# Performance work log

Hardware: AMD Instinct MI355X
Metric: run time of the kernel (lower is better)

Reference implementation:

```python
import jax, jax.numpy as jnp
import numpy as np

N_NODES = 50000
N_EDGES = 800000
D_IN = 64
D_OUT = 64


def setup_inputs() -> dict:
    key = jax.random.key(0)
    k1, k2, k3, k4, k5, k6 = jax.random.split(key, 6)
    stdv = 1.0 / np.sqrt(D_OUT)
    return {
        "X": jax.random.normal(k1, (N_NODES, D_IN), dtype=jnp.float32),
        "edge_src": jax.random.randint(k2, (N_EDGES,), 0, N_NODES, dtype=jnp.int32),
        "edge_dst": jax.random.randint(k3, (N_EDGES,), 0, N_NODES, dtype=jnp.int32),
        "edge_weight": jax.random.uniform(k4, (N_EDGES,), dtype=jnp.float32),
        "weight": jax.random.uniform(k5, (D_IN, D_OUT), jnp.float32, -stdv, stdv),
        "b": jax.random.uniform(k6, (D_OUT,), jnp.float32, -stdv, stdv),
    }


def reference(X, edge_src, edge_dst, edge_weight, weight, b):
    # support = X @ W                        [N, D_OUT]
    support = jnp.dot(X, weight)
    # spmm: out[d] = sum_{e: dst(e)=d} w_e * support[src(e)]
    messages = edge_weight[:, None] * support[edge_src]  # [E, D_OUT]
    output = jax.ops.segment_sum(messages, edge_dst, num_segments=N_NODES)
    return output + b
```

## Files before the change

kernel.cpp:

```cpp
#include <hip/hip_runtime.h>
#include <hip/hip_bf16.h>

#define N_NODES 50000
#define N_EDGES 800000
#define DIM     64
#define CAP     64

#define GEMM_BLOCKS ((N_NODES + 31) / 32)
#define FILL_BLOCKS ((N_EDGES / 4 + 255) / 256)
#define TOTAL_BLOCKS (GEMM_BLOCKS + FILL_BLOCKS)
#define INTERLEAVED  (2 * FILL_BLOCKS)

#define WS_SUPPORT  0
#define WS_CURSOR   6400000
#define WS_BUCKET   9600000

__device__ inline unsigned bf16_hi(float f) {
    const unsigned u = __float_as_uint(f);
    return (u + 0x7fffu + ((u >> 16) & 1u)) & 0xffff0000u;
}

__global__ __launch_bounds__(256) void fused_gemm_fill_kernel(
        const float* __restrict__ X,
        const float* __restrict__ W,
        ushort* __restrict__ support,
        const int*   __restrict__ edge_src,
        const int*   __restrict__ edge_dst,
        const float* __restrict__ edge_weight,
        int*      __restrict__ cursor,
        unsigned* __restrict__ bucket) {
    const int tid = threadIdx.x;

    if (blockIdx.x < INTERLEAVED && (blockIdx.x & 1) == 0) {
        const int bid  = blockIdx.x >> 1;
        const int base = (bid * 256 + tid) * 4;
        if (base < N_EDGES) {
            const int4   d = *(const int4*)  &edge_dst[base];
            const int4   s = *(const int4*)  &edge_src[base];
            const float4 w = *(const float4*)&edge_weight[base];
            const unsigned e0 = bf16_hi(w.x) | (unsigned)s.x;
            const unsigned e1 = bf16_hi(w.y) | (unsigned)s.y;
            const unsigned e2 = bf16_hi(w.z) | (unsigned)s.z;
            const unsigned e3 = bf16_hi(w.w) | (unsigned)s.w;
            const int p0 = atomicAdd(&cursor[d.x << 4], 1);
            const int p1 = atomicAdd(&cursor[d.y << 4], 1);
            const int p2 = atomicAdd(&cursor[d.z << 4], 1);
            const int p3 = atomicAdd(&cursor[d.w << 4], 1);
            if (p0 < CAP) bucket[d.x * CAP + p0] = e0;
            if (p1 < CAP) bucket[d.y * CAP + p1] = e1;
            if (p2 < CAP) bucket[d.z * CAP + p2] = e2;
            if (p3 < CAP) bucket[d.w * CAP + p3] = e3;
        }
        return;
    }

    __shared__ float sX[32 * 68];
    __shared__ float sW[64 * 64];
    const int bid = (blockIdx.x < INTERLEAVED) ? (blockIdx.x >> 1)
                                               : (blockIdx.x - FILL_BLOCKS);
    const int rowBase = bid * 32;

    #pragma unroll
    for (int i = 0; i < 2; ++i) {
        const int q   = tid + 256 * i;
        const int row = q >> 4;
        const int c4  = q & 15;
        float4 v = make_float4(0.f, 0.f, 0.f, 0.f);
        if (rowBase + row < N_NODES)
            v = *(const float4*)&X[(rowBase + row) * DIM + c4 * 4];
        *(float4*)&sX[row * 68 + c4 * 4] = v;
    }
    #pragma unroll
    for (int i = 0; i < 4; ++i) {
        const int q   = tid + 256 * i;
        const int row = q >> 4;
        const int c4  = q & 15;
        *(float4*)&sW[row * 64 + c4 * 4] = *(const float4*)&W[row * DIM + c4 * 4];
    }
    __syncthreads();

    const int tx = tid & 15;
    const int ty = tid >> 4;
    float acc[2][4];
    #pragma unroll
    for (int i = 0; i < 2; ++i)
        #pragma unroll
        for (int j = 0; j < 4; ++j) acc[i][j] = 0.f;

    #pragma unroll
    for (int k4 = 0; k4 < 16; ++k4) {
        float4 xv[2], wv[4];
        #pragma unroll
        for (int i = 0; i < 2; ++i)
            xv[i] = *(const float4*)&sX[(ty * 2 + i) * 68 + k4 * 4];
        #pragma unroll
        for (int kk = 0; kk < 4; ++kk)
            wv[kk] = *(const float4*)&sW[(k4 * 4 + kk) * 64 + tx * 4];
        #pragma unroll
        for (int i = 0; i < 2; ++i) {
            #pragma unroll
            for (int kk = 0; kk < 4; ++kk) {
                const float f = ((const float*)&xv[i])[kk];
                acc[i][0] += f * wv[kk].x;
                acc[i][1] += f * wv[kk].y;
                acc[i][2] += f * wv[kk].z;
                acc[i][3] += f * wv[kk].w;
            }
        }
    }

    #pragma unroll
    for (int i = 0; i < 2; ++i) {
        const int r = rowBase + ty * 2 + i;
        if (r < N_NODES) {
            ushort4 v;
            v.x = __hip_bfloat16_raw(__float2bfloat16(acc[i][0])).x;
            v.y = __hip_bfloat16_raw(__float2bfloat16(acc[i][1])).x;
            v.z = __hip_bfloat16_raw(__float2bfloat16(acc[i][2])).x;
            v.w = __hip_bfloat16_raw(__float2bfloat16(acc[i][3])).x;
            *(ushort4*)&support[r * DIM + tx * 4] = v;
        }
    }
}

__global__ __launch_bounds__(256) void gather_kernel(const int*      __restrict__ cursor,
                                                     const unsigned* __restrict__ bucket,
                                                     const unsigned* __restrict__ support32,
                                                     const float*    __restrict__ b,
                                                     float* __restrict__ out) {
    const int node = blockIdx.x * 4 + (threadIdx.x >> 6);
    const int lane = threadIdx.x & 63;
    const int half = lane >> 5;
    const int sub  = lane & 31;
    if (node >= N_NODES) return;

    int cnt = cursor[node << 4];
    if (cnt > CAP) cnt = CAP;
    const unsigned ent = bucket[node * CAP + lane];

    float acc0 = 0.f, acc1 = 0.f;
    int j = 0;
    for (; j + 8 <= cnt; j += 8) {
        unsigned e[4], u[4];
        #pragma unroll
        for (int k = 0; k < 4; ++k) e[k] = __shfl(ent, j + 2 * k + half);
        #pragma unroll
        for (int k = 0; k < 4; ++k) u[k] = support32[(e[k] & 0xffffu) * 32 + sub];
        #pragma unroll
        for (int k = 0; k < 4; ++k) {
            const float w = __uint_as_float(e[k] & 0xffff0000u);
            acc0 += w * __uint_as_float(u[k] << 16);
            acc1 += w * __uint_as_float(u[k] & 0xffff0000u);
        }
    }
    for (; j + 2 <= cnt; j += 2) {
        const unsigned e = __shfl(ent, j + half);
        const unsigned u = support32[(e & 0xffffu) * 32 + sub];
        const float    w = __uint_as_float(e & 0xffff0000u);
        acc0 += w * __uint_as_float(u << 16);
        acc1 += w * __uint_as_float(u & 0xffff0000u);
    }
    if (j < cnt) {
        const unsigned e = __shfl(ent, j);
        const unsigned u = support32[(e & 0xffffu) * 32 + sub];
        const float    w = half ? 0.f : __uint_as_float(e & 0xffff0000u);
        acc0 += w * __uint_as_float(u << 16);
        acc1 += w * __uint_as_float(u & 0xffff0000u);
    }

    acc0 += __shfl_xor(acc0, 32);
    acc1 += __shfl_xor(acc1, 32);

    if (half == 0) {
        const float2 bb = *(const float2*)&b[sub * 2];
        float2 o;
        o.x = acc0 + bb.x;
        o.y = acc1 + bb.y;
        *(float2*)&out[node * DIM + sub * 2] = o;
    }
}

extern "C" void kernel_launch(void* const* d_in, const int* in_sizes, int n_in,
                              void* d_out, int out_size, void* d_ws, size_t ws_size,
                              hipStream_t stream) {
    const float* X           = (const float*)d_in[0];
    const int*   edge_src    = (const int*)  d_in[1];
    const int*   edge_dst    = (const int*)  d_in[2];
    const float* edge_weight = (const float*)d_in[3];
    const float* W           = (const float*)d_in[4];
    const float* b           = (const float*)d_in[5];
    float*       out         = (float*)d_out;

    char* ws = (char*)d_ws;
    ushort*   support = (ushort*)  (ws + WS_SUPPORT);
    int*      cursor  = (int*)     (ws + WS_CURSOR);
    unsigned* bucket  = (unsigned*)(ws + WS_BUCKET);

    hipMemsetAsync(cursor, 0, N_NODES * 16 * sizeof(int), stream);

    hipLaunchKernelGGL(fused_gemm_fill_kernel, dim3(TOTAL_BLOCKS),
                       dim3(256), 0, stream,
                       X, W, support, edge_src, edge_dst, edge_weight,
                       cursor, bucket);

    hipLaunchKernelGGL(gather_kernel, dim3(N_NODES / 4), dim3(256), 0, stream,
                       cursor, bucket, (const unsigned*)support, b, out);
}
```

Measured before the change: 143.8 us.

## Merge memset, GEMM/fill and gather into one cooperative persistent kernel

Replaces the memset plus two kernel launches with a single cooperative kernel of 512 persistent blocks. The blocks zero the cursor array, grid-sync, loop over edge-fill chunks and 16-row GEMM tiles, grid-sync again, then run the gather. The cursor array is no longer padded to 64 bytes per node, so it shrinks and its atomics land on adjacent cache lines. The change removes launch gaps and tail effects, but adds the cost of grid-wide barriers, a fixed grid size that may underfill the GPU, and smaller GEMM tiles that reload W per block.

```diff
diff --git a/kernel.cpp b/kernel.cpp
--- a/kernel.cpp
+++ b/kernel.cpp
@@ -1,75 +1,51 @@
 #include <hip/hip_runtime.h>
+#include <hip/hip_cooperative_groups.h>
 #include <hip/hip_bf16.h>
+
+namespace cg = cooperative_groups;
 
 #define N_NODES 50000
 #define N_EDGES 800000
 #define DIM     64
 #define CAP     64
 
-#define GEMM_BLOCKS ((N_NODES + 31) / 32)
-#define FILL_BLOCKS ((N_EDGES / 4 + 255) / 256)
-#define TOTAL_BLOCKS (GEMM_BLOCKS + FILL_BLOCKS)
-#define INTERLEAVED  (2 * FILL_BLOCKS)
+#define GRID_BLOCKS  512
+#define FILL_CHUNKS  ((N_EDGES + 1023) / 1024)
+#define GEMM_TILES   (N_NODES / 16)
+#define PHASEA_WORK  (FILL_CHUNKS + GEMM_TILES)
+#define GATHER_GROUPS (N_NODES / 4)
 
-#define WS_SUPPORT  0
-#define WS_CURSOR   6400000
-#define WS_BUCKET   9600000
+#define WS_SUPPORT 0
+#define WS_CURSOR  6400000
+#define WS_BUCKET  6600192
 
 __device__ inline unsigned bf16_hi(float f) {
     const unsigned u = __float_as_uint(f);
     return (u + 0x7fffu + ((u >> 16) & 1u)) & 0xffff0000u;
 }
 
-__global__ __launch_bounds__(256) void fused_gemm_fill_kernel(
+__global__ __launch_bounds__(256) void mega_kernel(
         const float* __restrict__ X,
         const float* __restrict__ W,
-        ushort* __restrict__ support,
+        ushort*      __restrict__ support,
         const int*   __restrict__ edge_src,
         const int*   __restrict__ edge_dst,
         const float* __restrict__ edge_weight,
-        int*      __restrict__ cursor,
-        unsigned* __restrict__ bucket) {
+        int*         __restrict__ cursor,
+        unsigned*    __restrict__ bucket,
+        const float* __restrict__ b,
+        float*       __restrict__ out) {
+    cg::grid_group grid = cg::this_grid();
     const int tid = threadIdx.x;
 
-    if (blockIdx.x < INTERLEAVED && (blockIdx.x & 1) == 0) {
-        const int bid  = blockIdx.x >> 1;
-        const int base = (bid * 256 + tid) * 4;
-        if (base < N_EDGES) {
-            const int4   d = *(const int4*)  &edge_dst[base];
-            const int4   s = *(const int4*)  &edge_src[base];
-            const float4 w = *(const float4*)&edge_weight[base];
-            const unsigned e0 = bf16_hi(w.x) | (unsigned)s.x;
-            const unsigned e1 = bf16_hi(w.y) | (unsigned)s.y;
-            const unsigned e2 = bf16_hi(w.z) | (unsigned)s.z;
-            const unsigned e3 = bf16_hi(w.w) | (unsigned)s.w;
-            const int p0 = atomicAdd(&cursor[d.x << 4], 1);
-            const int p1 = atomicAdd(&cursor[d.y << 4], 1);
-            const int p2 = atomicAdd(&cursor[d.z << 4], 1);
-            const int p3 = atomicAdd(&cursor[d.w << 4], 1);
-            if (p0 < CAP) bucket[d.x * CAP + p0] = e0;
-            if (p1 < CAP) bucket[d.y * CAP + p1] = e1;
-            if (p2 < CAP) bucket[d.z * CAP + p2] = e2;
-            if (p3 < CAP) bucket[d.w * CAP + p3] = e3;
-        }
-        return;
+    {
+        const int i = blockIdx.x * 256 + tid;
+        if (i < N_NODES) cursor[i] = 0;
     }
+    grid.sync();
 
-    __shared__ float sX[32 * 68];
+    __shared__ float sX[16 * 68];
     __shared__ float sW[64 * 64];
-    const int bid = (blockIdx.x < INTERLEAVED) ? (blockIdx.x >> 1)
-                                               : (blockIdx.x - FILL_BLOCKS);
-    const int rowBase = bid * 32;
-
-    #pragma unroll
-    for (int i = 0; i < 2; ++i) {
-        const int q   = tid + 256 * i;
-        const int row = q >> 4;
-        const int c4  = q & 15;
-        float4 v = make_float4(0.f, 0.f, 0.f, 0.f);
-        if (rowBase + row < N_NODES)
-            v = *(const float4*)&X[(rowBase + row) * DIM + c4 * 4];
-        *(float4*)&sX[row * 68 + c4 * 4] = v;
-    }
     #pragma unroll
     for (int i = 0; i < 4; ++i) {
         const int q   = tid + 256 * i;
@@ -79,104 +55,115 @@
     }
     __syncthreads();
 
-    const int tx = tid & 15;
-    const int ty = tid >> 4;
-    float acc[2][4];
-    #pragma unroll
-    for (int i = 0; i < 2; ++i)
-        #pragma unroll
-        for (int j = 0; j < 4; ++j) acc[i][j] = 0.f;
+    for (int w = blockIdx.x; w < PHASEA_WORK; w += GRID_BLOCKS) {
+        if (w < FILL_CHUNKS) {
+            const int base = w * 1024 + tid * 4;
+            if (base < N_EDGES) {
+                const int4   d = *(const int4*)  &edge_dst[base];
+                const int4   s = *(const int4*)  &edge_src[base];
+                const float4 wt = *(const float4*)&edge_weight[base];
+                const unsigned e0 = bf16_hi(wt.x) | (unsigned)s.x;
+                const unsigned e1 = bf16_hi(wt.y) | (unsigned)s.y;
+                const unsigned e2 = bf16_hi(wt.z) | (unsigned)s.z;
+                const unsigned e3 = bf16_hi(wt.w) | (unsigned)s.w;
+                const int p0 = atomicAdd(&cursor[d.x], 1);
+                const int p1 = atomicAdd(&cursor[d.y], 1);
+                const int p2 = atomicAdd(&cursor[d.z], 1);
+                const int p3 = atomicAdd(&cursor[d.w], 1);
+                if (p0 < CAP) bucket[d.x * CAP + p0] = e0;
+                if (p1 < CAP) bucket[d.y * CAP + p1] = e1;
+                if (p2 < CAP) bucket[d.z * CAP + p2] = e2;
+                if (p3 < CAP) bucket[d.w * CAP + p3] = e3;
+            }
+        } else {
+            const int rowBase = (w - FILL_CHUNKS) * 16;
+            __syncthreads();
+            {
+                const int row = tid >> 4;
+                const int c4  = tid & 15;
+                *(float4*)&sX[row * 68 + c4 * 4] =
+                    *(const float4*)&X[(rowBase + row) * DIM + c4 * 4];
+            }
+            __syncthreads();
 
-    #pragma unroll
-    for (int k4 = 0; k4 < 16; ++k4) {
-        float4 xv[2], wv[4];
-        #pragma unroll
-        for (int i = 0; i < 2; ++i)
-            xv[i] = *(const float4*)&sX[(ty * 2 + i) * 68 + k4 * 4];
-        #pragma unroll
-        for (int kk = 0; kk < 4; ++kk)
-            wv[kk] = *(const float4*)&sW[(k4 * 4 + kk) * 64 + tx * 4];
-        #pragma unroll
-        for (int i = 0; i < 2; ++i) {
+            const int tx = tid & 15;
+            const int ty = tid >> 4;
+            float a0 = 0.f, a1 = 0.f, a2 = 0.f, a3 = 0.f;
             #pragma unroll
-            for (int kk = 0; kk < 4; ++kk) {
-                const float f = ((const float*)&xv[i])[kk];
-                acc[i][0] += f * wv[kk].x;
-                acc[i][1] += f * wv[kk].y;
-                acc[i][2] += f * wv[kk].z;
-                acc[i][3] += f * wv[kk].w;
+            for (int k4 = 0; k4 < 16; ++k4) {
+                const float4 xv = *(const float4*)&sX[ty * 68 + k4 * 4];
+                #pragma unroll
+                for (int kk = 0; kk < 4; ++kk) {
+                    const float4 wv = *(const float4*)&sW[(k4 * 4 + kk) * 64 + tx * 4];
+                    const float  f  = ((const float*)&xv)[kk];
+                    a0 += f * wv.x;
+                    a1 += f * wv.y;
+                    a2 += f * wv.z;
+                    a3 += f * wv.w;
+                }
+            }
+            ushort4 v;
+            v.x = __hip_bfloat16_raw(__float2bfloat16(a0)).x;
+            v.y = __hip_bfloat16_raw(__float2bfloat16(a1)).x;
+            v.z = __hip_bfloat16_raw(__float2bfloat16(a2)).x;
+            v.w = __hip_bfloat16_raw(__float2bfloat16(a3)).x;
+            *(ushort4*)&support[(rowBase + ty) * DIM + tx * 4] = v;
+        }
+    }
+    grid.sync();
+
+    const int lane = tid & 63;
+    const int half = lane >> 5;
+    const int sub  = lane & 31;
+    const unsigned* support32 = (const unsigned*)support;
+    const float2 bb = *(const float2*)&b[sub * 2];
+
+    for (int g = blockIdx.x; g < GATHER_GROUPS; g += GRID_BLOCKS) {
+        const int node = g * 4 + (tid >> 6);
+
+        int cnt = cursor[node];
+        if (cnt > CAP) cnt = CAP;
+        const unsigned ent = bucket[node * CAP + lane];
+
+        float acc0 = 0.f, acc1 = 0.f;
+        int j = 0;
+        for (; j + 8 <= cnt; j += 8) {
+            unsigned e[4], u[4];
+            #pragma unroll
+            for (int k = 0; k < 4; ++k) e[k] = __shfl(ent, j + 2 * k + half);
+            #pragma unroll
+            for (int k = 0; k < 4; ++k) u[k] = support32[(e[k] & 0xffffu) * 32 + sub];
+            #pragma unroll
+            for (int k = 0; k < 4; ++k) {
+                const float w2 = __uint_as_float(e[k] & 0xffff0000u);
+                acc0 += w2 * __uint_as_float(u[k] << 16);
+                acc1 += w2 * __uint_as_float(u[k] & 0xffff0000u);
             }
         }
-    }
+        for (; j + 2 <= cnt; j += 2) {
+            const unsigned e = __shfl(ent, j + half);
+            const unsigned u = support32[(e & 0xffffu) * 32 + sub];
+            const float    w2 = __uint_as_float(e & 0xffff0000u);
+            acc0 += w2 * __uint_as_float(u << 16);
+            acc1 += w2 * __uint_as_float(u & 0xffff0000u);
+        }
+        if (j < cnt) {
+            const unsigned e = __shfl(ent, j);
+            const unsigned u = support32[(e & 0xffffu) * 32 + sub];
+            const float    w2 = half ? 0.f : __uint_as_float(e & 0xffff0000u);
+            acc0 += w2 * __uint_as_float(u << 16);
+            acc1 += w2 * __uint_as_float(u & 0xffff0000u);
+        }
 
-    #pragma unroll
-    for (int i = 0; i < 2; ++i) {
-        const int r = rowBase + ty * 2 + i;
-        if (r < N_NODES) {
-            ushort4 v;
-            v.x = __hip_bfloat16_raw(__float2bfloat16(acc[i][0])).x;
-            v.y = __hip_bfloat16_raw(__float2bfloat16(acc[i][1])).x;
-            v.z = __hip_bfloat16_raw(__float2bfloat16(acc[i][2])).x;
-            v.w = __hip_bfloat16_raw(__float2bfloat16(acc[i][3])).x;
-            *(ushort4*)&support[r * DIM + tx * 4] = v;
+        acc0 += __shfl_xor(acc0, 32);
+        acc1 += __shfl_xor(acc1, 32);
+
+        if (half == 0) {
+            float2 o;
+            o.x = acc0 + bb.x;
+            o.y = acc1 + bb.y;
+            *(float2*)&out[node * DIM + sub * 2] = o;
         }
-    }
-}
-
-__global__ __launch_bounds__(256) void gather_kernel(const int*      __restrict__ cursor,
-                                                     const unsigned* __restrict__ bucket,
-                                                     const unsigned* __restrict__ support32,
-                                                     const float*    __restrict__ b,
-                                                     float* __restrict__ out) {
-    const int node = blockIdx.x * 4 + (threadIdx.x >> 6);
-    const int lane = threadIdx.x & 63;
-    const int half = lane >> 5;
-    const int sub  = lane & 31;
-    if (node >= N_NODES) return;
-
-    int cnt = cursor[node << 4];
-    if (cnt > CAP) cnt = CAP;
-    const unsigned ent = bucket[node * CAP + lane];
-
-    float acc0 = 0.f, acc1 = 0.f;
-    int j = 0;
-    for (; j + 8 <= cnt; j += 8) {
-        unsigned e[4], u[4];
-        #pragma unroll
-        for (int k = 0; k < 4; ++k) e[k] = __shfl(ent, j + 2 * k + half);
-        #pragma unroll
-        for (int k = 0; k < 4; ++k) u[k] = support32[(e[k] & 0xffffu) * 32 + sub];
-        #pragma unroll
-        for (int k = 0; k < 4; ++k) {
-            const float w = __uint_as_float(e[k] & 0xffff0000u);
-            acc0 += w * __uint_as_float(u[k] << 16);
-            acc1 += w * __uint_as_float(u[k] & 0xffff0000u);
-        }
-    }
-    for (; j + 2 <= cnt; j += 2) {
-        const unsigned e = __shfl(ent, j + half);
-        const unsigned u = support32[(e & 0xffffu) * 32 + sub];
-        const float    w = __uint_as_float(e & 0xffff0000u);
-        acc0 += w * __uint_as_float(u << 16);
-        acc1 += w * __uint_as_float(u & 0xffff0000u);
-    }
-    if (j < cnt) {
-        const unsigned e = __shfl(ent, j);
-        const unsigned u = support32[(e & 0xffffu) * 32 + sub];
-        const float    w = half ? 0.f : __uint_as_float(e & 0xffff0000u);
-        acc0 += w * __uint_as_float(u << 16);
-        acc1 += w * __uint_as_float(u & 0xffff0000u);
-    }
-
-    acc0 += __shfl_xor(acc0, 32);
-    acc1 += __shfl_xor(acc1, 32);
-
-    if (half == 0) {
-        const float2 bb = *(const float2*)&b[sub * 2];
-        float2 o;
-        o.x = acc0 + bb.x;
-        o.y = acc1 + bb.y;
-        *(float2*)&out[node * DIM + sub * 2] = o;
     }
 }
 
@@ -196,13 +183,10 @@
     int*      cursor  = (int*)     (ws + WS_CURSOR);
     unsigned* bucket  = (unsigned*)(ws + WS_BUCKET);
 
-    hipMemsetAsync(cursor, 0, N_NODES * 16 * sizeof(int), stream);
+    void* args[] = { (void*)&X, (void*)&W, (void*)&support,
+                     (void*)&edge_src, (void*)&edge_dst, (void*)&edge_weight,
+                     (void*)&cursor, (void*)&bucket, (void*)&b, (void*)&out };
 
-    hipLaunchKernelGGL(fused_gemm_fill_kernel, dim3(TOTAL_BLOCKS),
-                       dim3(256), 0, stream,
-                       X, W, support, edge_src, edge_dst, edge_weight,
-                       cursor, bucket);
-
-    hipLaunchKernelGGL(gather_kernel, dim3(N_NODES / 4), dim3(256), 0, stream,
-                       cursor, bucket, (const unsigned*)support, b, out);
+    hipLaunchCooperativeKernel((void*)mega_kernel, dim3(GRID_BLOCKS), dim3(256),
+                               args, 0, stream);
 }
```

Result: slower. 278.9 us (+93.9%).
